# Performance work log

Hardware: AMD Instinct MI355X
Metric: run time of the kernel (lower is better)

Reference implementation:

```python
import jax, jax.numpy as jnp
import numpy as np

TAU = 0.5  # config.tau
EPS = 1e-12  # F.normalize eps


def _pair_idx(n_i, hi):
    # all pairs (i, j) with i in [0, n_i), j in (i, hi)
    ii, jj = [], []
    for i in range(n_i):
        js = np.arange(i + 1, hi)
        ii.append(np.full(js.shape, i))
        jj.append(js)
    return np.concatenate(ii), np.concatenate(jj)


def setup_inputs() -> dict:
    key = jax.random.key(0)
    ks = jax.random.split(key, 7)
    B, D, H = 512, 768, 256
    s = 0.02
    return {
        "emb_in": jax.random.normal(ks[0], (B, D), jnp.float32),
        "W1": jax.random.normal(ks[1], (H, 2 * D), jnp.float32) * s,
        "b1": jax.random.normal(ks[2], (H,), jnp.float32) * s,
        "W2": jax.random.normal(ks[3], (H, H), jnp.float32) * s,
        "b2": jax.random.normal(ks[4], (H,), jnp.float32) * s,
        "W3": jax.random.normal(ks[5], (1, H), jnp.float32) * s,
        "b3": jax.random.normal(ks[6], (1,), jnp.float32) * s,
    }


def reference(emb_in, W1, b1, W2, b2, W3, b3):
    B, D = emb_in.shape
    n = B // 4
    m = B // 2

    # L2 normalize rows (torch F.normalize)
    z = emb_in / jnp.maximum(jnp.linalg.norm(emb_in, axis=1, keepdims=True), EPS)
    # cosine similarity matrix [B, B]
    S = z @ z.T

    # ---- ContrastiveLoss (NT-Xent style over first n rows) ----
    logits = S / jnp.asarray(TAU, emb_in.dtype)
    not_diag = 1.0 - jnp.eye(B, dtype=emb_in.dtype)
    denom = jnp.sum(not_diag * jnp.exp(logits), axis=1)  # sum_{k != i} exp(S[i,k]/T)
    log_denom = jnp.log(denom)  # [B]
    ci, cj = _pair_idx(n, n)  # pairs i < j < n
    # loss_ij = -log( exp(S[i,j]/T) / denom_i ) = log_denom[i] - logits[i, j]
    closs_sum = jnp.sum(log_denom[ci] - logits[ci, cj])
    closs = (-2.0 * (n - 1) / n) * closs_sum

    # ---- en_loss: pairwise concat + tiny MLP + BCEWithLogits ----
    ei_np, ej_np = _pair_idx(n, B)  # pairs i in [0,n), j in (i, B)
    ei = jnp.asarray(ei_np)
    ej = jnp.asarray(ej_np)
    labels = (ej_np < m).astype(np.float32)  # first m-(i+1) pairs per i are positives
    labels = jnp.asarray(labels)

    x = jnp.concatenate([z[ei], z[ej]], axis=1)  # [P, 2D]
    h1 = jax.nn.relu(x @ W1.T + b1)              # [P, H]
    h2 = jax.nn.relu(h1 @ W2.T + b2)             # [P, H]
    logit = (h2 @ W3.T + b3)[:, 0]               # [P]

    # BCEWithLogitsLoss (mean), numerically stable form
    bce = jnp.maximum(logit, 0.0) - logit * labels + jnp.log1p(jnp.exp(-jnp.abs(logit)))
    eloss = jnp.mean(bce)

    return closs + eloss
```

## Files before the change

kernel.cpp:

```cpp
#include <hip/hip_runtime.h>
#include <hip/hip_bf16.h>
#include <math.h>

#define B 512
#define D 768
#define H 256
#define NN 128
#define MM 256
#define P_PAIRS 57280
#define NPBLK 895

typedef __attribute__((ext_vector_type(8))) __bf16 bf16x8;
typedef __attribute__((ext_vector_type(4))) __bf16 bf16x4;
typedef __attribute__((ext_vector_type(4))) float f32x4;


__global__ __launch_bounds__(256) void k_prep(const float* __restrict__ emb,
                                              const float* __restrict__ W1,
                                              const float* __restrict__ W2,
                                              __bf16* __restrict__ zA,
                                              __bf16* __restrict__ W1A,
                                              __bf16* __restrict__ W2s) {
    int bx = blockIdx.x;
    int t = threadIdx.x;
    if (bx < B) {
        int i = bx;
        float4 v4 = make_float4(0.f, 0.f, 0.f, 0.f);
        float ss = 0.f;
        if (t < D / 4) {
            v4 = *(const float4*)(emb + i * D + 4 * t);
            ss = v4.x * v4.x + v4.y * v4.y + v4.z * v4.z + v4.w * v4.w;
        }
        __shared__ float red[256];
        red[t] = ss;
        __syncthreads();
        for (int s = 128; s > 0; s >>= 1) {
            if (t < s) red[t] += red[t + s];
            __syncthreads();
        }
        float inv = 1.0f / fmaxf(sqrtf(red[0]), 1e-12f);
        if (t < D / 4) {
            bf16x4 o;
            o[0] = (__bf16)(v4.x * inv); o[1] = (__bf16)(v4.y * inv);
            o[2] = (__bf16)(v4.z * inv); o[3] = (__bf16)(v4.w * inv);
            int g = i >> 4, r = i & 15;
            int s24 = t >> 3, q = (t >> 1) & 3, e = (t & 1) * 4;
            *(bf16x4*)(zA + (((g * 24 + s24) * 64 + q * 16 + r) * 8 + e)) = o;
        }
    } else if (bx < B + 64) {
        int n = (bx - B) * 4 + (t >> 6);
        int c = t & 63;
        float4 w = *(const float4*)(W2 + n * H + 4 * c);
        bf16x4 o;
        o[0] = (__bf16)w.x; o[1] = (__bf16)w.y; o[2] = (__bf16)w.z; o[3] = (__bf16)w.w;
        int g = n >> 4, r = n & 15;
        int s8 = c >> 3, q = (c >> 1) & 3, e = (c & 1) * 4;
        *(bf16x4*)(W2s + (((g * 8 + s8) * 64 + q * 16 + r) * 8 + e)) = o;
    } else {
        int n = bx - B - 64;
        if (t < D / 4) {
            float4 w = *(const float4*)(W1 + (n & 255) * (2 * D) + (n >> 8) * D + 4 * t);
            bf16x4 o;
            o[0] = (__bf16)w.x; o[1] = (__bf16)w.y; o[2] = (__bf16)w.z; o[3] = (__bf16)w.w;
            int g = n >> 4, r = n & 15;
            int s24 = t >> 3, q = (t >> 1) & 3, e = (t & 1) * 4;
            *(bf16x4*)(W1A + (((g * 24 + s24) * 64 + q * 16 + r) * 8 + e)) = o;
        }
    }
}

__global__ __launch_bounds__(128) void k_sim_uv(const __bf16* __restrict__ zA,
                                                const __bf16* __restrict__ W1A,
                                                const float* __restrict__ b1,
                                                __bf16* __restrict__ Up,
                                                __bf16* __restrict__ Vv,
                                                float* __restrict__ esp,
                                                float* __restrict__ slp) {
    int bx = blockIdx.x;
    int w = threadIdx.x >> 6;
    int lane = threadIdx.x & 63;
    int r = lane & 15, q = lane >> 4;

    if (bx < 32) {
        int gm = bx >> 2;
        int gn0 = (bx & 3) * 8 + w * 4;
        int slot = (bx & 3) * 2 + w;
        f32x4 acc[4] = {};
        #pragma unroll 4
        for (int s = 0; s < D / 32; s++) {
            bf16x8 a = *(const bf16x8*)(zA + ((gm * 24 + s) * 64 + lane) * 8);
            #pragma unroll
            for (int nt = 0; nt < 4; nt++) {
                bf16x8 b = *(const bf16x8*)(zA + (((gn0 + nt) * 24 + s) * 64 + lane) * 8);
                acc[nt] = __builtin_amdgcn_mfma_f32_16x16x32_bf16(a, b, acc[nt], 0, 0, 0);
            }
        }
        #pragma unroll
        for (int rr = 0; rr < 4; rr++) {
            int irow = gm * 16 + q * 4 + rr;
            float es = 0.f, sl = 0.f;
            #pragma unroll
            for (int nt = 0; nt < 4; nt++) {
                int kcol = (gn0 + nt) * 16 + r;
                float C = acc[nt][rr];
                if (kcol != irow) es += expf(2.f * C);
                if (kcol > irow && kcol < NN) sl += 2.f * C;
            }
            #pragma unroll
            for (int m = 1; m <= 8; m <<= 1) {
                es += __shfl_xor(es, m);
                sl += __shfl_xor(sl, m);
            }
            if (r == 0) {
                esp[slot * NN + irow] = es;
                slp[slot * NN + irow] = sl;
            }
        }
    } else {
        int bxu = bx - 32;
        int gm = (bxu >> 3) * 2 + w;
        int gn0 = (bxu & 7) * 4;
        f32x4 acc[4] = {};
        #pragma unroll 4
        for (int s = 0; s < D / 32; s++) {
            bf16x8 a = *(const bf16x8*)(zA + ((gm * 24 + s) * 64 + lane) * 8);
            #pragma unroll
            for (int nt = 0; nt < 4; nt++) {
                bf16x8 b = *(const bf16x8*)(W1A + (((gn0 + nt) * 24 + s) * 64 + lane) * 8);
                acc[nt] = __builtin_amdgcn_mfma_f32_16x16x32_bf16(a, b, acc[nt], 0, 0, 0);
            }
        }
        #pragma unroll
        for (int nt = 0; nt < 4; nt++) {
            int n = (gn0 + nt) * 16 + r;
            float bias = (n < H) ? b1[n] : 0.f;
            #pragma unroll
            for (int rr = 0; rr < 4; rr++) {
                int m = gm * 16 + 4 * q + rr;
                float C = acc[nt][rr] + bias;
                if (n < H) Up[m * H + n] = (__bf16)C;
                else       Vv[m * H + (n - H)] = (__bf16)C;
            }
        }
    }
}

__global__ __launch_bounds__(256, 4) void k_pairs(const __bf16* __restrict__ Up,
                                                  const __bf16* __restrict__ Vv,
                                                  const __bf16* __restrict__ W2s,
                                                  const float* __restrict__ b2,
                                                  const float* __restrict__ W3,
                                                  const float* __restrict__ b3,
                                                  float* __restrict__ bcepart) {
    __shared__ __bf16 h1[64][264];
    __shared__ int jj_s[64];
    __shared__ float redbuf[4][64];

    int tid = threadIdx.x;
    int w = tid >> 6, lane = tid & 63;
    int r = lane & 15, q = lane >> 4;
    int p0 = blockIdx.x * 64;

    if (tid < 64) {
        int p = p0 + tid;
        float disc = 1046529.f - 8.f * (float)p;
        int i = (int)((1023.f - sqrtf(disc)) * 0.5f);
        if (i < 0) i = 0;
        if (i > NN - 1) i = NN - 1;
        while (i > 0 && i * (1023 - i) / 2 > p) i--;
        while ((i + 1) * (1022 - i) / 2 <= p) i++;
        int j = i + 1 + (p - i * (1023 - i) / 2);
        jj_s[tid] = (i << 16) | j;
    }
    __syncthreads();

    {
        int row = tid >> 2;
        int cq = tid & 3;
        int ij = jj_s[row];
        int i = ij >> 16, j = ij & 0xffff;
        const __bf16* up = Up + i * H + 64 * cq;
        const __bf16* vp = Vv + j * H + 64 * cq;
        #pragma unroll
        for (int c8 = 0; c8 < 8; c8++) {
            bf16x8 u8 = *(const bf16x8*)(up + 8 * c8);
            bf16x8 v8 = *(const bf16x8*)(vp + 8 * c8);
            bf16x8 hv;
            #pragma unroll
            for (int e = 0; e < 8; e++)
                hv[e] = (__bf16)fmaxf((float)u8[e] + (float)v8[e], 0.f);
            *(bf16x8*)&h1[row][64 * cq + 8 * c8] = hv;
        }
    }
    __syncthreads();

    f32x4 acc[4][4] = {};
    #pragma unroll
    for (int s = 0; s < 8; s++) {
        bf16x8 a[4], b[4];
        #pragma unroll
        for (int mt = 0; mt < 4; mt++)
            a[mt] = *(const bf16x8*)&h1[16 * mt + r][32 * s + 8 * q];
        #pragma unroll
        for (int nt = 0; nt < 4; nt++)
            b[nt] = *(const bf16x8*)(W2s + (((4 * w + nt) * 8 + s) * 64 + lane) * 8);
        #pragma unroll
        for (int mt = 0; mt < 4; mt++)
            #pragma unroll
            for (int nt = 0; nt < 4; nt++)
                acc[mt][nt] = __builtin_amdgcn_mfma_f32_16x16x32_bf16(a[mt], b[nt], acc[mt][nt], 0, 0, 0);
    }

    float part[4][4] = {};
    #pragma unroll
    for (int nt = 0; nt < 4; nt++) {
        int n = 64 * w + 16 * nt + r;
        float b2v = b2[n], w3v = W3[n];
        #pragma unroll
        for (int mt = 0; mt < 4; mt++)
            #pragma unroll
            for (int rr = 0; rr < 4; rr++) {
                float h2 = fmaxf(acc[mt][nt][rr] + b2v, 0.f);
                part[mt][rr] += h2 * w3v;
            }
    }
    #pragma unroll
    for (int mt = 0; mt < 4; mt++)
        #pragma unroll
        for (int rr = 0; rr < 4; rr++) {
            float v = part[mt][rr];
            #pragma unroll
            for (int m = 1; m <= 8; m <<= 1) v += __shfl_xor(v, m);
            if (r == 0) redbuf[w][16 * mt + 4 * q + rr] = v;
        }
    __syncthreads();

    if (tid < 64) {
        int j = jj_s[tid] & 0xffff;
        float logit = redbuf[0][tid] + redbuf[1][tid] +
                      redbuf[2][tid] + redbuf[3][tid] + b3[0];
        float label = (j < MM) ? 1.f : 0.f;
        float lsum = fmaxf(logit, 0.f) - logit * label +
                     log1pf(expf(-fabsf(logit)));
        #pragma unroll
        for (int off = 32; off > 0; off >>= 1) lsum += __shfl_down(lsum, off);
        if (tid == 0) bcepart[blockIdx.x] = lsum;
    }
}

__global__ __launch_bounds__(256) void k_final(const float* __restrict__ esp,
                                               const float* __restrict__ slp,
                                               const float* __restrict__ bcepart,
                                               float* __restrict__ out) {
    __shared__ float red[256];
    int t = threadIdx.x;

    float s = 0.f;
    for (int p = t; p < NPBLK; p += 256) s += bcepart[p];
    red[t] = s;
    __syncthreads();
    for (int st = 128; st > 0; st >>= 1) {
        if (t < st) red[t] += red[t + st];
        __syncthreads();
    }
    float bce_total = red[0];
    __syncthreads();

    float v = 0.f;
    if (t < NN) {
        float es = 0.f, sl = 0.f;
        #pragma unroll
        for (int s8 = 0; s8 < 8; s8++) {
            es += esp[s8 * NN + t];
            sl += slp[s8 * NN + t];
        }
        v = (float)(NN - 1 - t) * logf(es) - sl;
    }
    red[t] = v;
    __syncthreads();
    for (int st = 128; st > 0; st >>= 1) {
        if (t < st) red[t] += red[t + st];
        __syncthreads();
    }
    if (t == 0) {
        float closs = (-2.0f * (float)(NN - 1) / (float)NN) * red[0];
        out[0] = closs + bce_total / (float)P_PAIRS;
    }
}

extern "C" void kernel_launch(void* const* d_in, const int* in_sizes, int n_in,
                              void* d_out, int out_size, void* d_ws, size_t ws_size,
                              hipStream_t stream) {
    const float* emb = (const float*)d_in[0];
    const float* W1  = (const float*)d_in[1];
    const float* b1  = (const float*)d_in[2];
    const float* W2  = (const float*)d_in[3];
    const float* b2  = (const float*)d_in[4];
    const float* W3  = (const float*)d_in[5];
    const float* b3  = (const float*)d_in[6];
    float* out = (float*)d_out;

    float* ws = (float*)d_ws;
    float* esp     = ws;
    float* slp     = ws + 1024;
    float* bcepart = ws + 2048;
    __bf16* zA  = (__bf16*)(ws + 3072);
    __bf16* W1A = zA + B * D;
    __bf16* W2s = W1A + 2 * H * D;
    __bf16* Up  = W2s + H * H;
    __bf16* Vv  = Up + B * H;

    k_prep<<<B + 64 + 2 * H, 256, 0, stream>>>(emb, W1, W2, zA, W1A, W2s);
    k_sim_uv<<<160, 128, 0, stream>>>(zA, W1A, b1, Up, Vv, esp, slp);
    k_pairs<<<NPBLK, 256, 0, stream>>>(Up, Vv, W2s, b2, W3, b3, bcepart);
    k_final<<<1, 256, 0, stream>>>(esp, slp, bcepart, out);
}
```

Baseline: 103.2 us.

## Switch to fp16, enlarge pair tiles, move similarity into pairs kernel

Changes every operand from bf16 to fp16 and uses packed fp16 add/max to build h1. The pairs kernel now takes 128 pairs per block, which halves the block count and doubles reuse of the W2 fragments loaded per block, at the cost of more accumulators and lower occupancy. The similarity/NT-Xent partial sums move into extra blocks of the pairs kernel, leaving a dedicated UV GEMM kernel with finer tiles. The prep kernel is restructured into 80 blocks that write 16-byte vectors. fp16 has less exponent range than bf16, but normalized and small-weight values should stay in range.

```diff
diff --git a/kernel.cpp b/kernel.cpp
--- a/kernel.cpp
+++ b/kernel.cpp
@@ -8,91 +8,151 @@
 #define NN 128
 #define MM 256
 #define P_PAIRS 57280
-#define NPBLK 895
-
-typedef __attribute__((ext_vector_type(8))) __bf16 bf16x8;
-typedef __attribute__((ext_vector_type(4))) __bf16 bf16x4;
-typedef __attribute__((ext_vector_type(4))) float f32x4;
+#define NPBLK_P 448
+
+typedef _Float16 f16x8 __attribute__((ext_vector_type(8)));
+typedef _Float16 f16x4 __attribute__((ext_vector_type(4)));
+typedef float f32x4 __attribute__((ext_vector_type(4)));
 
 
 __global__ __launch_bounds__(256) void k_prep(const float* __restrict__ emb,
                                               const float* __restrict__ W1,
                                               const float* __restrict__ W2,
-                                              __bf16* __restrict__ zA,
-                                              __bf16* __restrict__ W1A,
-                                              __bf16* __restrict__ W2s) {
+                                              _Float16* __restrict__ zH,
+                                              _Float16* __restrict__ W1H,
+                                              _Float16* __restrict__ W2H) {
     int bx = blockIdx.x;
-    int t = threadIdx.x;
-    if (bx < B) {
-        int i = bx;
-        float4 v4 = make_float4(0.f, 0.f, 0.f, 0.f);
-        float ss = 0.f;
-        if (t < D / 4) {
-            v4 = *(const float4*)(emb + i * D + 4 * t);
-            ss = v4.x * v4.x + v4.y * v4.y + v4.z * v4.z + v4.w * v4.w;
-        }
-        __shared__ float red[256];
-        red[t] = ss;
+    int tid = threadIdx.x;
+    int w = tid >> 6, lane = tid & 63;
+
+    if (bx < 32) {
+        int g = bx;
+        __shared__ float invs[16];
+        for (int rr = 0; rr < 4; rr++) {
+            int row = 16 * g + 4 * w + rr;
+            const float* rp = emb + row * D;
+            float ss = 0.f;
+            #pragma unroll
+            for (int it = 0; it < 12; it++) {
+                float v = rp[lane + 64 * it];
+                ss += v * v;
+            }
+            #pragma unroll
+            for (int m = 1; m <= 32; m <<= 1) ss += __shfl_xor(ss, m);
+            if (lane == 0) invs[4 * w + rr] = 1.0f / fmaxf(sqrtf(ss), 1e-12f);
+        }
         __syncthreads();
-        for (int s = 128; s > 0; s >>= 1) {
-            if (t < s) red[t] += red[t + s];
-            __syncthreads();
-        }
-        float inv = 1.0f / fmaxf(sqrtf(red[0]), 1e-12f);
-        if (t < D / 4) {
-            bf16x4 o;
-            o[0] = (__bf16)(v4.x * inv); o[1] = (__bf16)(v4.y * inv);
-            o[2] = (__bf16)(v4.z * inv); o[3] = (__bf16)(v4.w * inv);
-            int g = i >> 4, r = i & 15;
-            int s24 = t >> 3, q = (t >> 1) & 3, e = (t & 1) * 4;
-            *(bf16x4*)(zA + (((g * 24 + s24) * 64 + q * 16 + r) * 8 + e)) = o;
-        }
-    } else if (bx < B + 64) {
-        int n = (bx - B) * 4 + (t >> 6);
-        int c = t & 63;
-        float4 w = *(const float4*)(W2 + n * H + 4 * c);
-        bf16x4 o;
-        o[0] = (__bf16)w.x; o[1] = (__bf16)w.y; o[2] = (__bf16)w.z; o[3] = (__bf16)w.w;
-        int g = n >> 4, r = n & 15;
-        int s8 = c >> 3, q = (c >> 1) & 3, e = (c & 1) * 4;
-        *(bf16x4*)(W2s + (((g * 8 + s8) * 64 + q * 16 + r) * 8 + e)) = o;
+        for (int it = 0; it < 6; it++) {
+            int chunk = it * 256 + tid;
+            int s = chunk >> 6, lc = chunk & 63;
+            int q = lc >> 4, r = lc & 15;
+            const float* src = emb + (16 * g + r) * D + 32 * s + 8 * q;
+            float inv = invs[r];
+            float4 a = *(const float4*)src;
+            float4 b = *(const float4*)(src + 4);
+            f16x8 o;
+            o[0] = (_Float16)(a.x * inv); o[1] = (_Float16)(a.y * inv);
+            o[2] = (_Float16)(a.z * inv); o[3] = (_Float16)(a.w * inv);
+            o[4] = (_Float16)(b.x * inv); o[5] = (_Float16)(b.y * inv);
+            o[6] = (_Float16)(b.z * inv); o[7] = (_Float16)(b.w * inv);
+            *(f16x8*)(zH + ((g * 24 + s) * 64 + lc) * 8) = o;
+        }
+    } else if (bx < 64) {
+        int g = bx - 32;
+        for (int it = 0; it < 6; it++) {
+            int chunk = it * 256 + tid;
+            int s = chunk >> 6, lc = chunk & 63;
+            int q = lc >> 4, r = lc & 15;
+            int n = 16 * g + r;
+            const float* src = W1 + (n & 255) * (2 * D) + (n >> 8) * D + 32 * s + 8 * q;
+            float4 a = *(const float4*)src;
+            float4 b = *(const float4*)(src + 4);
+            f16x8 o;
+            o[0] = (_Float16)a.x; o[1] = (_Float16)a.y; o[2] = (_Float16)a.z; o[3] = (_Float16)a.w;
+            o[4] = (_Float16)b.x; o[5] = (_Float16)b.y; o[6] = (_Float16)b.z; o[7] = (_Float16)b.w;
+            *(f16x8*)(W1H + ((g * 24 + s) * 64 + lc) * 8) = o;
+        }
     } else {
-        int n = bx - B - 64;
-        if (t < D / 4) {
-            float4 w = *(const float4*)(W1 + (n & 255) * (2 * D) + (n >> 8) * D + 4 * t);
-            bf16x4 o;
-            o[0] = (__bf16)w.x; o[1] = (__bf16)w.y; o[2] = (__bf16)w.z; o[3] = (__bf16)w.w;
-            int g = n >> 4, r = n & 15;
-            int s24 = t >> 3, q = (t >> 1) & 3, e = (t & 1) * 4;
-            *(bf16x4*)(W1A + (((g * 24 + s24) * 64 + q * 16 + r) * 8 + e)) = o;
-        }
-    }
-}
-
-__global__ __launch_bounds__(128) void k_sim_uv(const __bf16* __restrict__ zA,
-                                                const __bf16* __restrict__ W1A,
-                                                const float* __restrict__ b1,
-                                                __bf16* __restrict__ Up,
-                                                __bf16* __restrict__ Vv,
-                                                float* __restrict__ esp,
-                                                float* __restrict__ slp) {
-    int bx = blockIdx.x;
+        int g = bx - 64;
+        for (int it = 0; it < 2; it++) {
+            int chunk = it * 256 + tid;
+            int s = chunk >> 6, lc = chunk & 63;
+            int q = lc >> 4, r = lc & 15;
+            const float* src = W2 + (16 * g + r) * H + 32 * s + 8 * q;
+            float4 a = *(const float4*)src;
+            float4 b = *(const float4*)(src + 4);
+            f16x8 o;
+            o[0] = (_Float16)a.x; o[1] = (_Float16)a.y; o[2] = (_Float16)a.z; o[3] = (_Float16)a.w;
+            o[4] = (_Float16)b.x; o[5] = (_Float16)b.y; o[6] = (_Float16)b.z; o[7] = (_Float16)b.w;
+            *(f16x8*)(W2H + ((g * 8 + s) * 64 + lc) * 8) = o;
+        }
+    }
+}
+
+__global__ __launch_bounds__(256) void k_uv(const _Float16* __restrict__ zH,
+                                            const _Float16* __restrict__ W1H,
+                                            const float* __restrict__ b1,
+                                            _Float16* __restrict__ Up,
+                                            _Float16* __restrict__ Vv) {
     int w = threadIdx.x >> 6;
     int lane = threadIdx.x & 63;
     int r = lane & 15, q = lane >> 4;
-
-    if (bx < 32) {
-        int gm = bx >> 2;
-        int gn0 = (bx & 3) * 8 + w * 4;
-        int slot = (bx & 3) * 2 + w;
+    int tile = blockIdx.x * 4 + w;
+    int gm = tile >> 4;
+    int gnp = tile & 15;
+
+    f32x4 acc[2] = {};
+    #pragma unroll 4
+    for (int s = 0; s < 24; s++) {
+        f16x8 a = *(const f16x8*)(zH + ((gm * 24 + s) * 64 + lane) * 8);
+        #pragma unroll
+        for (int nt = 0; nt < 2; nt++) {
+            f16x8 b = *(const f16x8*)(W1H + (((gnp * 2 + nt) * 24 + s) * 64 + lane) * 8);
+            acc[nt] = __builtin_amdgcn_mfma_f32_16x16x32_f16(a, b, acc[nt], 0, 0, 0);
+        }
+    }
+    #pragma unroll
+    for (int nt = 0; nt < 2; nt++) {
+        int n = (gnp * 2 + nt) * 16 + r;
+        float bias = (n < H) ? b1[n] : 0.f;
+        #pragma unroll
+        for (int rr = 0; rr < 4; rr++) {
+            int m = gm * 16 + 4 * q + rr;
+            float C = acc[nt][rr] + bias;
+            if (n < H) Up[m * H + n] = (_Float16)C;
+            else       Vv[m * H + (n - H)] = (_Float16)C;
+        }
+    }
+}
+
+__global__ __launch_bounds__(256, 2) void k_pairs(const _Float16* __restrict__ Up,
+                                                  const _Float16* __restrict__ Vv,
+                                                  const _Float16* __restrict__ W2H,
+                                                  const _Float16* __restrict__ zH,
+                                                  const float* __restrict__ b2,
+                                                  const float* __restrict__ W3,
+                                                  const float* __restrict__ b3,
+                                                  float* __restrict__ bcepart,
+                                                  float* __restrict__ esp,
+                                                  float* __restrict__ slp) {
+    int tid = threadIdx.x;
+    int w = tid >> 6, lane = tid & 63;
+    int r = lane & 15, q = lane >> 4;
+    int bx = blockIdx.x;
+
+    if (bx >= NPBLK_P) {
+        int t = (bx - NPBLK_P) * 4 + w;
+        int gm = t >> 3;
+        int slot = t & 7;
+        int gn0 = slot * 4;
         f32x4 acc[4] = {};
         #pragma unroll 4
-        for (int s = 0; s < D / 32; s++) {
-            bf16x8 a = *(const bf16x8*)(zA + ((gm * 24 + s) * 64 + lane) * 8);
+        for (int s = 0; s < 24; s++) {
+            f16x8 a = *(const f16x8*)(zH + ((gm * 24 + s) * 64 + lane) * 8);
             #pragma unroll
             for (int nt = 0; nt < 4; nt++) {
-                bf16x8 b = *(const bf16x8*)(zA + (((gn0 + nt) * 24 + s) * 64 + lane) * 8);
-                acc[nt] = __builtin_amdgcn_mfma_f32_16x16x32_bf16(a, b, acc[nt], 0, 0, 0);
+                f16x8 b = *(const f16x8*)(zH + (((gn0 + nt) * 24 + s) * 64 + lane) * 8);
+                acc[nt] = __builtin_amdgcn_mfma_f32_16x16x32_f16(a, b, acc[nt], 0, 0, 0);
             }
         }
         #pragma unroll
@@ -116,53 +176,18 @@
                 slp[slot * NN + irow] = sl;
             }
         }
-    } else {
-        int bxu = bx - 32;
-        int gm = (bxu >> 3) * 2 + w;
-        int gn0 = (bxu & 7) * 4;
-        f32x4 acc[4] = {};
-        #pragma unroll 4
-        for (int s = 0; s < D / 32; s++) {
-            bf16x8 a = *(const bf16x8*)(zA + ((gm * 24 + s) * 64 + lane) * 8);
-            #pragma unroll
-            for (int nt = 0; nt < 4; nt++) {
-                bf16x8 b = *(const bf16x8*)(W1A + (((gn0 + nt) * 24 + s) * 64 + lane) * 8);
-                acc[nt] = __builtin_amdgcn_mfma_f32_16x16x32_bf16(a, b, acc[nt], 0, 0, 0);
-            }
-        }
-        #pragma unroll
-        for (int nt = 0; nt < 4; nt++) {
-            int n = (gn0 + nt) * 16 + r;
-            float bias = (n < H) ? b1[n] : 0.f;
-            #pragma unroll
-            for (int rr = 0; rr < 4; rr++) {
-                int m = gm * 16 + 4 * q + rr;
-                float C = acc[nt][rr] + bias;
-                if (n < H) Up[m * H + n] = (__bf16)C;
-                else       Vv[m * H + (n - H)] = (__bf16)C;
-            }
-        }
-    }
-}
-
-__global__ __launch_bounds__(256, 4) void k_pairs(const __bf16* __restrict__ Up,
-                                                  const __bf16* __restrict__ Vv,
-                                                  const __bf16* __restrict__ W2s,
-                                                  const float* __restrict__ b2,
-                                                  const float* __restrict__ W3,
-                                                  const float* __restrict__ b3,
-                                                  float* __restrict__ bcepart) {
-    __shared__ __bf16 h1[64][264];
-    __shared__ int jj_s[64];
-    __shared__ float redbuf[4][64];
-
-    int tid = threadIdx.x;
-    int w = tid >> 6, lane = tid & 63;
-    int r = lane & 15, q = lane >> 4;
-    int p0 = blockIdx.x * 64;
-
-    if (tid < 64) {
+        return;
+    }
+
+    __shared__ _Float16 h1[128][264];
+    __shared__ int jj_s[128];
+    __shared__ float redbuf[4][128];
+    __shared__ float red2[2];
+
+    int p0 = bx * 128;
+    if (tid < 128) {
         int p = p0 + tid;
+        if (p >= P_PAIRS) p = P_PAIRS - 1;
         float disc = 1046529.f - 8.f * (float)p;
         int i = (int)((1023.f - sqrtf(disc)) * 0.5f);
         if (i < 0) i = 0;
@@ -175,77 +200,85 @@
     __syncthreads();
 
     {
-        int row = tid >> 2;
-        int cq = tid & 3;
-        int ij = jj_s[row];
-        int i = ij >> 16, j = ij & 0xffff;
-        const __bf16* up = Up + i * H + 64 * cq;
-        const __bf16* vp = Vv + j * H + 64 * cq;
-        #pragma unroll
-        for (int c8 = 0; c8 < 8; c8++) {
-            bf16x8 u8 = *(const bf16x8*)(up + 8 * c8);
-            bf16x8 v8 = *(const bf16x8*)(vp + 8 * c8);
-            bf16x8 hv;
-            #pragma unroll
-            for (int e = 0; e < 8; e++)
-                hv[e] = (__bf16)fmaxf((float)u8[e] + (float)v8[e], 0.f);
-            *(bf16x8*)&h1[row][64 * cq + 8 * c8] = hv;
-        }
-    }
-    __syncthreads();
-
-    f32x4 acc[4][4] = {};
+        #pragma unroll
+        for (int uu = 0; uu < 2; uu++) {
+            int u = uu * 256 + tid;
+            int row = u >> 2, cq = u & 3;
+            int ij = jj_s[row];
+            int i = ij >> 16, j = ij & 0xffff;
+            const _Float16* up = Up + i * H + 64 * cq;
+            const _Float16* vp = Vv + j * H + 64 * cq;
+            #pragma unroll
+            for (int c8 = 0; c8 < 8; c8++) {
+                f16x8 u8 = *(const f16x8*)(up + 8 * c8);
+                f16x8 v8 = *(const f16x8*)(vp + 8 * c8);
+                f16x8 zero = {};
+                f16x8 hv = __builtin_elementwise_max(u8 + v8, zero);
+                *(f16x8*)&h1[row][64 * cq + 8 * c8] = hv;
+            }
+        }
+    }
+    __syncthreads();
+
+    f32x4 acc[8][4] = {};
     #pragma unroll
     for (int s = 0; s < 8; s++) {
-        bf16x8 a[4], b[4];
-        #pragma unroll
-        for (int mt = 0; mt < 4; mt++)
-            a[mt] = *(const bf16x8*)&h1[16 * mt + r][32 * s + 8 * q];
+        f16x8 b[4];
         #pragma unroll
         for (int nt = 0; nt < 4; nt++)
-            b[nt] = *(const bf16x8*)(W2s + (((4 * w + nt) * 8 + s) * 64 + lane) * 8);
-        #pragma unroll
-        for (int mt = 0; mt < 4; mt++)
+            b[nt] = *(const f16x8*)(W2H + (((4 * w + nt) * 8 + s) * 64 + lane) * 8);
+        #pragma unroll
+        for (int mt = 0; mt < 8; mt++) {
+            f16x8 a = *(const f16x8*)&h1[16 * mt + r][32 * s + 8 * q];
             #pragma unroll
             for (int nt = 0; nt < 4; nt++)
-                acc[mt][nt] = __builtin_amdgcn_mfma_f32_16x16x32_bf16(a[mt], b[nt], acc[mt][nt], 0, 0, 0);
-    }
-
-    float part[4][4] = {};
+                acc[mt][nt] = __builtin_amdgcn_mfma_f32_16x16x32_f16(a, b[nt], acc[mt][nt], 0, 0, 0);
+        }
+    }
+
+    float b2v[4], w3v[4];
     #pragma unroll
     for (int nt = 0; nt < 4; nt++) {
         int n = 64 * w + 16 * nt + r;
-        float b2v = b2[n], w3v = W3[n];
-        #pragma unroll
-        for (int mt = 0; mt < 4; mt++)
+        b2v[nt] = b2[n];
+        w3v[nt] = W3[n];
+    }
+    #pragma unroll
+    for (int mt = 0; mt < 8; mt++) {
+        float part[4] = {0.f, 0.f, 0.f, 0.f};
+        #pragma unroll
+        for (int nt = 0; nt < 4; nt++)
             #pragma unroll
             for (int rr = 0; rr < 4; rr++) {
-                float h2 = fmaxf(acc[mt][nt][rr] + b2v, 0.f);
-                part[mt][rr] += h2 * w3v;
-            }
-    }
-    #pragma unroll
-    for (int mt = 0; mt < 4; mt++)
+                float h2 = fmaxf(acc[mt][nt][rr] + b2v[nt], 0.f);
+                part[rr] += h2 * w3v[nt];
+            }
         #pragma unroll
         for (int rr = 0; rr < 4; rr++) {
-            float v = part[mt][rr];
+            float v = part[rr];
             #pragma unroll
             for (int m = 1; m <= 8; m <<= 1) v += __shfl_xor(v, m);
             if (r == 0) redbuf[w][16 * mt + 4 * q + rr] = v;
         }
-    __syncthreads();
-
-    if (tid < 64) {
+    }
+    __syncthreads();
+
+    if (tid < 128) {
+        int p = p0 + tid;
         int j = jj_s[tid] & 0xffff;
-        float logit = redbuf[0][tid] + redbuf[1][tid] +
-                      redbuf[2][tid] + redbuf[3][tid] + b3[0];
-        float label = (j < MM) ? 1.f : 0.f;
-        float lsum = fmaxf(logit, 0.f) - logit * label +
-                     log1pf(expf(-fabsf(logit)));
+        float lsum = 0.f;
+        if (p < P_PAIRS) {
+            float logit = redbuf[0][tid] + redbuf[1][tid] +
+                          redbuf[2][tid] + redbuf[3][tid] + b3[0];
+            float label = (j < MM) ? 1.f : 0.f;
+            lsum = fmaxf(logit, 0.f) - logit * label + log1pf(expf(-fabsf(logit)));
+        }
         #pragma unroll
         for (int off = 32; off > 0; off >>= 1) lsum += __shfl_down(lsum, off);
-        if (tid == 0) bcepart[blockIdx.x] = lsum;
-    }
+        if ((tid & 63) == 0) red2[tid >> 6] = lsum;
+    }
+    __syncthreads();
+    if (tid == 0) bcepart[bx] = red2[0] + red2[1];
 }
 
 __global__ __launch_bounds__(256) void k_final(const float* __restrict__ esp,
@@ -256,7 +289,7 @@
     int t = threadIdx.x;
 
     float s = 0.f;
-    for (int p = t; p < NPBLK; p += 256) s += bcepart[p];
+    for (int p = t; p < NPBLK_P; p += 256) s += bcepart[p];
     red[t] = s;
     __syncthreads();
     for (int st = 128; st > 0; st >>= 1) {
@@ -304,14 +337,15 @@
     float* esp     = ws;
     float* slp     = ws + 1024;
     float* bcepart = ws + 2048;
-    __bf16* zA  = (__bf16*)(ws + 3072);
-    __bf16* W1A = zA + B * D;
-    __bf16* W2s = W1A + 2 * H * D;
-    __bf16* Up  = W2s + H * H;
-    __bf16* Vv  = Up + B * H;
-
-    k_prep<<<B + 64 + 2 * H, 256, 0, stream>>>(emb, W1, W2, zA, W1A, W2s);
-    k_sim_uv<<<160, 128, 0, stream>>>(zA, W1A, b1, Up, Vv, esp, slp);
-    k_pairs<<<NPBLK, 256, 0, stream>>>(Up, Vv, W2s, b2, W3, b3, bcepart);
+    _Float16* zH  = (_Float16*)(ws + 2560);
+    _Float16* W1H = zH + B * D;
+    _Float16* W2H = W1H + 2 * H * D;
+    _Float16* Up  = W2H + H * H;
+    _Float16* Vv  = Up + B * H;
+
+    k_prep<<<80, 256, 0, stream>>>(emb, W1, W2, zH, W1H, W2H);
+    k_uv<<<128, 256, 0, stream>>>(zH, W1H, b1, Up, Vv);
+    k_pairs<<<NPBLK_P + 16, 256, 0, stream>>>(Up, Vv, W2H, zH, b2, W3, b3,
+                                              bcepart, esp, slp);
     k_final<<<1, 256, 0, stream>>>(esp, slp, bcepart, out);
 }
```

After: 101.3 us. About the same (-1.9%).
